# Kernel optimization log

Hardware: AMD Instinct MI355X
Metric: run time of the kernel (lower is better)

The kernel has to match this reference:

```python
import jax, jax.numpy as jnp
import numpy as np

NUM_QUANTIZERS = 8
CODEBOOK_SIZE = 4096
DIM = 128
BATCH = 8
SEQ = 4096


def setup_inputs() -> dict:
    key = jax.random.key(0)
    k1, k2 = jax.random.split(key)
    x = jax.random.normal(k1, (BATCH, DIM, SEQ), dtype=jnp.float32)
    codebooks = jax.random.normal(k2, (NUM_QUANTIZERS, CODEBOOK_SIZE, DIM), dtype=jnp.float32)
    return {"x": x, "codebooks": codebooks}


def _rvq(x_bnc, codebooks):
    """Residual VQ: sequential per-stage nearest-codebook quantization.

    x_bnc: [b, n, d]; codebooks: [Q, K, d].
    Returns quantized [b, n, d], indices [b, n, Q], loss scalar.
    """
    residual = x_bnc
    quantized_out = jnp.zeros_like(x_bnc)
    all_indices = []
    all_losses = []
    Q = codebooks.shape[0]
    for q in range(Q):
        cb = codebooks[q]                                   # [K, d]
        # squared-euclidean distances: ||r||^2 - 2 r.c + ||c||^2  -> [b, n, K]
        r_sq = jnp.sum(residual * residual, axis=-1, keepdims=True)
        c_sq = jnp.sum(cb * cb, axis=-1)
        dots = jnp.einsum('bnd,kd->bnk', residual, cb)
        dist = r_sq - 2.0 * dots + c_sq
        idx = jnp.argmin(dist, axis=-1)                      # [b, n]
        quant = cb[idx]                                      # [b, n, d] gather
        # straight-through estimator (grad flows to residual, not codebook)
        quant_st = residual + jax.lax.stop_gradient(quant - residual)
        quantized_out = quantized_out + quant_st
        # commitment loss (codebook is EMA-updated, so detach the quantized side)
        all_losses.append(jnp.mean((jax.lax.stop_gradient(quant) - residual) ** 2))
        residual = residual - jax.lax.stop_gradient(quant)
        all_indices.append(idx)
    indices = jnp.stack(all_indices, axis=-1)                # [b, n, Q]
    loss = jnp.mean(jnp.stack(all_losses))
    return quantized_out, indices, loss


def reference(x, codebooks):
    # encode(): 'b c n -> b n c', quantize, 'b n c -> b c n'
    x_bnc = jnp.transpose(x, (0, 2, 1))
    quant, indices, loss = _rvq(x_bnc, codebooks)
    out = jnp.transpose(quant, (0, 2, 1))                    # [b, c, n]
    return out, indices, loss
```

## Files before the change

kernel.cpp:

```cpp
#include <hip/hip_runtime.h>

typedef _Float16 half8 __attribute__((ext_vector_type(8)));
typedef float    float4v __attribute__((ext_vector_type(4)));

#define NQ 8
#define KCODES 4096
#define DIMS 128
#define BATCH 8
#define SEQ 4096
#define ROWS (BATCH*SEQ)
#define TM 64
#define NBLK (ROWS/TM)
#define RESPAD 132
#define CANDW 96
#define CANDPAD 100
#define OUT_ELEMS (BATCH*DIMS*SEQ)
#define IDX_ELEMS (BATCH*SEQ*NQ)
#define LOSS_DIV (1.0f/33554432.0f)
#define FRAG_HALVES ((size_t)NQ*4*256*64*8)
#define SBIAS 384.0f
#define WIN 2.0f

__device__ __forceinline__ unsigned umax_(unsigned a, unsigned b){ return a>b?a:b; }
__device__ __forceinline__ unsigned umin_(unsigned a, unsigned b){ return a<b?a:b; }

__global__ void prep_csq(const float* __restrict__ cb, float* __restrict__ csq,
                         float* __restrict__ cinit) {
    int c = blockIdx.x * 256 + threadIdx.x;
    const float4* p = (const float4*)(cb + (size_t)c * DIMS);
    float s = 0.f;
#pragma unroll
    for (int i = 0; i < 32; ++i) {
        float4 v = p[i];
        s += v.x * v.x + v.y * v.y + v.z * v.z + v.w * v.w;
    }
    csq[c] = s;
    cinit[c] = SBIAS - 0.5f * s;
}

__global__ void prep_frags(const float* __restrict__ cb, _Float16* __restrict__ bhi,
                           float* __restrict__ loss_accum) {
    int g = blockIdx.x * 256 + threadIdx.x;
    if (g == 0) loss_accum[0] = 0.f;
    int lane = g & 63;
    int nt   = (g >> 6) & 255;
    int kb   = (g >> 14) & 3;
    int q    = g >> 16;
    int code = nt * 16 + (lane & 15);
    int k0   = kb * 32 + ((lane >> 4) * 8);
    const float* src = cb + ((size_t)q * KCODES + code) * DIMS + k0;
    float4 v0 = *(const float4*)(src);
    float4 v1 = *(const float4*)(src + 4);
    half8 h;
    h[0] = (_Float16)v0.x; h[1] = (_Float16)v0.y; h[2] = (_Float16)v0.z; h[3] = (_Float16)v0.w;
    h[4] = (_Float16)v1.x; h[5] = (_Float16)v1.y; h[6] = (_Float16)v1.z; h[7] = (_Float16)v1.w;
    *(half8*)(bhi + (size_t)g * 8) = h;
}

__device__ __forceinline__ void load_b(const _Float16* __restrict__ bq,
                                       const float* __restrict__ cinq,
                                       int nt, int lane, half8 (&bh)[4], float& cs) {
#pragma unroll
    for (int kb = 0; kb < 4; ++kb) {
        size_t off = (((size_t)kb * 256 + nt) * 64 + lane) * 8;
        bh[kb] = *(const half8*)(bq + off);
    }
    cs = cinq[nt * 16 + (lane & 15)];
}

__device__ __forceinline__ void compute_tile(int nt, int lane,
        const half8 (&ahi)[4][4], const half8 (&bh)[4], float cs,
        unsigned (&p1)[4][4], unsigned (&p2)[4][4], unsigned (&p3)[4][4]) {
    float4v acc[4];
#pragma unroll
    for (int mt = 0; mt < 4; ++mt) { acc[mt][0] = cs; acc[mt][1] = cs; acc[mt][2] = cs; acc[mt][3] = cs; }
    __builtin_amdgcn_s_setprio(1);
#pragma unroll
    for (int kb = 0; kb < 4; ++kb)
#pragma unroll
        for (int mt = 0; mt < 4; ++mt)
            acc[mt] = __builtin_amdgcn_mfma_f32_16x16x32_f16(ahi[mt][kb], bh[kb], acc[mt], 0, 0, 0);
    __builtin_amdgcn_s_setprio(0);
    unsigned idxv = (unsigned)(nt * 16 + (lane & 15));
#pragma unroll
    for (int mt = 0; mt < 4; ++mt)
#pragma unroll
        for (int r = 0; r < 4; ++r) {
            unsigned p  = (__float_as_uint(acc[mt][r]) & 0xFFFFF000u) | idxv;
            unsigned t1 = umin_(p1[mt][r], p);
            p1[mt][r]   = umax_(p1[mt][r], p);
            unsigned t2 = umin_(p2[mt][r], t1);
            p2[mt][r]   = umax_(p2[mt][r], t1);
            p3[mt][r]   = umax_(p3[mt][r], t2);
        }
}

__launch_bounds__(256, 2)
__global__ void rvq_main(const float* __restrict__ x, const float* __restrict__ cb,
                         const _Float16* __restrict__ bhi,
                         const float* __restrict__ csq, const float* __restrict__ cinit,
                         float* __restrict__ out, float* __restrict__ loss_accum) {
    __shared__ float    res[TM][RESPAD];
    __shared__ unsigned cand[TM][CANDPAD];
    __shared__ float    fbin[TM];
    __shared__ float    red[256];

    int tid  = threadIdx.x;
    int lane = tid & 63;
    int wv   = tid >> 6;
    int r0   = blockIdx.x * TM;
    int b    = r0 >> 12;
    int n0   = r0 & (SEQ - 1);
    const float* xb = x + (size_t)b * DIMS * SEQ + n0;

    {
        int d = tid >> 1, half = (tid & 1) * 32;
        const float* src = xb + (size_t)d * SEQ + half;
#pragma unroll
        for (int t4 = 0; t4 < 8; ++t4) {
            float4 v = *(const float4*)(src + t4 * 4);
            res[half + t4 * 4 + 0][d] = v.x;
            res[half + t4 * 4 + 1][d] = v.y;
            res[half + t4 * 4 + 2][d] = v.z;
            res[half + t4 * 4 + 3][d] = v.w;
        }
    }

    float lossacc = 0.f;

    for (int q = 0; q < NQ; ++q) {
        __syncthreads();

        half8 ahi[4][4];
#pragma unroll
        for (int mt = 0; mt < 4; ++mt)
#pragma unroll
        for (int kb = 0; kb < 4; ++kb) {
            int row = mt * 16 + (lane & 15);
            int k0  = kb * 32 + (lane >> 4) * 8;
            float4 v0 = *(const float4*)&res[row][k0];
            float4 v1 = *(const float4*)&res[row][k0 + 4];
            half8 h;
            h[0] = (_Float16)v0.x; h[1] = (_Float16)v0.y; h[2] = (_Float16)v0.z; h[3] = (_Float16)v0.w;
            h[4] = (_Float16)v1.x; h[5] = (_Float16)v1.y; h[6] = (_Float16)v1.z; h[7] = (_Float16)v1.w;
            ahi[mt][kb] = h;
        }

        const _Float16* bq   = bhi + (size_t)q * (4 * 256 * 64 * 8);
        const float*    cinq = cinit + q * KCODES;
        const float*    csqq = csq + q * KCODES;

        unsigned p1[4][4], p2[4][4], p3[4][4];
#pragma unroll
        for (int mt = 0; mt < 4; ++mt)
#pragma unroll
        for (int r = 0; r < 4; ++r) { p1[mt][r] = 0u; p2[mt][r] = 0u; p3[mt][r] = 0u; }

        int ntBase = wv * 64;
        half8 bh0[4], bh1[4];
        float cs0, cs1;
        load_b(bq, cinq, ntBase, lane, bh0, cs0);

        if (wv & 1) {
            float4v accD[4];
#pragma unroll
            for (int mt = 0; mt < 4; ++mt) { accD[mt][0] = cs0; accD[mt][1] = cs0; accD[mt][2] = cs0; accD[mt][3] = cs0; }
            __builtin_amdgcn_s_setprio(1);
#pragma unroll
            for (int kb = 0; kb < 3; ++kb)
#pragma unroll
                for (int mt = 0; mt < 4; ++mt)
                    accD[mt] = __builtin_amdgcn_mfma_f32_16x16x32_f16(ahi[mt][kb], bh0[kb], accD[mt], 0, 0, 0);
            __builtin_amdgcn_s_setprio(0);
            lossacc = fmaf(0.0f, (accD[0][0] + accD[1][0]) + (accD[2][0] + accD[3][0]), lossacc);
        }

        for (int i = 0; i < 64; i += 2) {
            load_b(bq, cinq, ntBase + i + 1, lane, bh1, cs1);
            compute_tile(ntBase + i, lane, ahi, bh0, cs0, p1, p2, p3);
            load_b(bq, cinq, ntBase + ((i + 2) & 63), lane, bh0, cs0);
            compute_tile(ntBase + i + 1, lane, ahi, bh1, cs1, p1, p2, p3);
        }

#pragma unroll
        for (int mt = 0; mt < 4; ++mt)
#pragma unroll
        for (int r = 0; r < 4; ++r) {
            unsigned a1 = p1[mt][r], a2 = p2[mt][r], a3 = p3[mt][r];
            unsigned b1 = (unsigned)__shfl_xor((int)a1, 1, 64);
            unsigned b2 = (unsigned)__shfl_xor((int)a2, 1, 64);
            unsigned b3 = (unsigned)__shfl_xor((int)a3, 1, 64);
            unsigned h  = umax_(a1, b1);
            unsigned l  = umin_(a1, b1);
            unsigned y  = umax_(a2, b2);
            unsigned n2 = umax_(l, y);
            unsigned n3 = umax_(umin_(l, y), umax_(a3, b3));
            if ((lane & 1) == 0) {
                int row = mt * 16 + (lane >> 4) * 4 + r;
                int col = wv * 24 + ((lane & 15) >> 1) * 3;
                cand[row][col]     = h;
                cand[row][col + 1] = n2;
                cand[row][col + 2] = n3;
            }
        }
        __syncthreads();

        {
            int row = tid >> 2, s = tid & 3;
            const unsigned* cp = &cand[row][s * 24];
            unsigned m = 0;
#pragma unroll
            for (int k = 0; k < 24; ++k) m = umax_(m, cp[k]);
            m = umax_(m, (unsigned)__shfl_xor((int)m, 1, 64));
            m = umax_(m, (unsigned)__shfl_xor((int)m, 2, 64));
            float thr = __uint_as_float(m) - WIN;
            float bk = -3.4e38f;
            int   bi = KCODES;
            const float4* rv = (const float4*)&res[row][0];
            for (int k = 0; k < 24; ++k) {
                unsigned e = cp[k];
                if (__uint_as_float(e) >= thr) {
                    int idx = (int)(e & 0xFFFu);
                    const float4* cv = (const float4*)(cb + ((size_t)q * KCODES + idx) * DIMS);
                    float acc = 0.f;
#pragma unroll
                    for (int j = 0; j < 32; ++j) {
                        float4 c4 = cv[j];
                        float4 r4 = rv[j];
                        acc = fmaf(r4.x, c4.x, acc);
                        acc = fmaf(r4.y, c4.y, acc);
                        acc = fmaf(r4.z, c4.z, acc);
                        acc = fmaf(r4.w, c4.w, acc);
                    }
                    float key = acc - 0.5f * csqq[idx];
                    if (key > bk || (key == bk && idx < bi)) { bk = key; bi = idx; }
                }
            }
#pragma unroll
            for (int mask = 1; mask <= 2; mask <<= 1) {
                float ok = __shfl_xor(bk, mask, 64);
                int   oi = __shfl_xor(bi, mask, 64);
                if (ok > bk || (ok == bk && oi < bi)) { bk = ok; bi = oi; }
            }
            if (s == 0) {
                fbin[row] = (float)bi;
                out[OUT_ELEMS + (size_t)(r0 + row) * NQ + q] = (float)bi;
            }
        }
        __syncthreads();

        {
            int row = tid >> 2, j = tid & 3;
            int bi = (int)fbin[row];
            const float* cv = cb + ((size_t)q * KCODES + bi) * DIMS + j * 4;
            float* rp = &res[row][j * 4];
#pragma unroll
            for (int t = 0; t < 8; ++t) {
                float4 c4 = *(const float4*)(cv + t * 16);
                float4 r4 = *(const float4*)(rp + t * 16);
                r4.x -= c4.x; lossacc = fmaf(r4.x, r4.x, lossacc);
                r4.y -= c4.y; lossacc = fmaf(r4.y, r4.y, lossacc);
                r4.z -= c4.z; lossacc = fmaf(r4.z, r4.z, lossacc);
                r4.w -= c4.w; lossacc = fmaf(r4.w, r4.w, lossacc);
                *(float4*)(rp + t * 16) = r4;
            }
        }
    }

    __syncthreads();
    red[tid] = lossacc;
    __syncthreads();
    for (int s = 128; s > 0; s >>= 1) {
        if (tid < s) red[tid] += red[tid + s];
        __syncthreads();
    }
    if (tid == 0) atomicAdd(loss_accum, red[0]);

    {
        int d = tid >> 1, half = (tid & 1) * 32;
        const float* src = xb + (size_t)d * SEQ + half;
        float* dst = out + (size_t)b * DIMS * SEQ + (size_t)d * SEQ + n0 + half;
#pragma unroll
        for (int t4 = 0; t4 < 8; ++t4) {
            float4 v = *(const float4*)(src + t4 * 4);
            v.x -= res[half + t4 * 4 + 0][d];
            v.y -= res[half + t4 * 4 + 1][d];
            v.z -= res[half + t4 * 4 + 2][d];
            v.w -= res[half + t4 * 4 + 3][d];
            *(float4*)(dst + t4 * 4) = v;
        }
    }
}

__global__ void finish_loss(const float* __restrict__ loss_accum, float* __restrict__ out) {
    out[OUT_ELEMS + IDX_ELEMS] = loss_accum[0] * LOSS_DIV;
}

extern "C" void kernel_launch(void* const* d_in, const int* in_sizes, int n_in,
                              void* d_out, int out_size, void* d_ws, size_t ws_size,
                              hipStream_t stream) {
    const float* x  = (const float*)d_in[0];
    const float* cb = (const float*)d_in[1];
    float* out = (float*)d_out;
    char*  ws  = (char*)d_ws;

    float*     loss_accum = (float*)ws;
    float*     csq   = (float*)(ws + 256);
    float*     cinit = (float*)(ws + 256 + 131072);
    _Float16*  bhi   = (_Float16*)(ws + 256 + 262144);

    hipLaunchKernelGGL(prep_csq,   dim3(128),  dim3(256), 0, stream, cb, csq, cinit);
    hipLaunchKernelGGL(prep_frags, dim3(2048), dim3(256), 0, stream, cb, bhi, loss_accum);
    hipLaunchKernelGGL(rvq_main,   dim3(NBLK), dim3(256), 0, stream,
                       x, cb, bhi, csq, cinit, out, loss_accum);
    hipLaunchKernelGGL(finish_loss, dim3(1), dim3(1), 0, stream, loss_accum, out);
}
```

Before: 565.9 us.

## Keep top-2 fp16 candidates per lane and raise occupancy to three blocks

```diff
diff --git a/kernel.cpp b/kernel.cpp
--- a/kernel.cpp
+++ b/kernel.cpp
@@ -12,8 +12,7 @@
 #define TM 64
 #define NBLK (ROWS/TM)
 #define RESPAD 132
-#define CANDW 96
-#define CANDPAD 100
+#define CANDROW 67
 #define OUT_ELEMS (BATCH*DIMS*SEQ)
 #define IDX_ELEMS (BATCH*SEQ*NQ)
 #define LOSS_DIV (1.0f/33554432.0f)
@@ -70,7 +69,7 @@
 
 __device__ __forceinline__ void compute_tile(int nt, int lane,
         const half8 (&ahi)[4][4], const half8 (&bh)[4], float cs,
-        unsigned (&p1)[4][4], unsigned (&p2)[4][4], unsigned (&p3)[4][4]) {
+        unsigned (&p1)[4][4], unsigned (&p2)[4][4]) {
     float4v acc[4];
 #pragma unroll
     for (int mt = 0; mt < 4; ++mt) { acc[mt][0] = cs; acc[mt][1] = cs; acc[mt][2] = cs; acc[mt][3] = cs; }
@@ -89,19 +88,17 @@
             unsigned p  = (__float_as_uint(acc[mt][r]) & 0xFFFFF000u) | idxv;
             unsigned t1 = umin_(p1[mt][r], p);
             p1[mt][r]   = umax_(p1[mt][r], p);
-            unsigned t2 = umin_(p2[mt][r], t1);
             p2[mt][r]   = umax_(p2[mt][r], t1);
-            p3[mt][r]   = umax_(p3[mt][r], t2);
-        }
-}
-
-__launch_bounds__(256, 2)
+        }
+}
+
+__launch_bounds__(256, 3)
 __global__ void rvq_main(const float* __restrict__ x, const float* __restrict__ cb,
                          const _Float16* __restrict__ bhi,
                          const float* __restrict__ csq, const float* __restrict__ cinit,
                          float* __restrict__ out, float* __restrict__ loss_accum) {
     __shared__ float    res[TM][RESPAD];
-    __shared__ unsigned cand[TM][CANDPAD];
+    __shared__ unsigned cand[TM][CANDROW];
     __shared__ float    fbin[TM];
     __shared__ float    red[256];
 
@@ -150,11 +147,11 @@
         const float*    cinq = cinit + q * KCODES;
         const float*    csqq = csq + q * KCODES;
 
-        unsigned p1[4][4], p2[4][4], p3[4][4];
+        unsigned p1[4][4], p2[4][4];
 #pragma unroll
         for (int mt = 0; mt < 4; ++mt)
 #pragma unroll
-        for (int r = 0; r < 4; ++r) { p1[mt][r] = 0u; p2[mt][r] = 0u; p3[mt][r] = 0u; }
+        for (int r = 0; r < 4; ++r) { p1[mt][r] = 0u; p2[mt][r] = 0u; }
 
         int ntBase = wv * 64;
         half8 bh0[4], bh1[4];
@@ -177,47 +174,42 @@
 
         for (int i = 0; i < 64; i += 2) {
             load_b(bq, cinq, ntBase + i + 1, lane, bh1, cs1);
-            compute_tile(ntBase + i, lane, ahi, bh0, cs0, p1, p2, p3);
+            compute_tile(ntBase + i, lane, ahi, bh0, cs0, p1, p2);
             load_b(bq, cinq, ntBase + ((i + 2) & 63), lane, bh0, cs0);
-            compute_tile(ntBase + i + 1, lane, ahi, bh1, cs1, p1, p2, p3);
+            compute_tile(ntBase + i + 1, lane, ahi, bh1, cs1, p1, p2);
         }
 
 #pragma unroll
         for (int mt = 0; mt < 4; ++mt)
 #pragma unroll
         for (int r = 0; r < 4; ++r) {
-            unsigned a1 = p1[mt][r], a2 = p2[mt][r], a3 = p3[mt][r];
+            unsigned a1 = p1[mt][r], a2 = p2[mt][r];
             unsigned b1 = (unsigned)__shfl_xor((int)a1, 1, 64);
             unsigned b2 = (unsigned)__shfl_xor((int)a2, 1, 64);
-            unsigned b3 = (unsigned)__shfl_xor((int)a3, 1, 64);
-            unsigned h  = umax_(a1, b1);
-            unsigned l  = umin_(a1, b1);
-            unsigned y  = umax_(a2, b2);
-            unsigned n2 = umax_(l, y);
-            unsigned n3 = umax_(umin_(l, y), umax_(a3, b3));
+            unsigned n1 = umax_(a1, b1);
+            unsigned n2 = umax_(umin_(a1, b1), umax_(a2, b2));
             if ((lane & 1) == 0) {
                 int row = mt * 16 + (lane >> 4) * 4 + r;
-                int col = wv * 24 + ((lane & 15) >> 1) * 3;
-                cand[row][col]     = h;
+                int col = wv * 16 + ((lane & 15) >> 1) * 2;
+                cand[row][col]     = n1;
                 cand[row][col + 1] = n2;
-                cand[row][col + 2] = n3;
             }
         }
         __syncthreads();
 
         {
             int row = tid >> 2, s = tid & 3;
-            const unsigned* cp = &cand[row][s * 24];
+            const unsigned* cp = &cand[row][s * 16];
             unsigned m = 0;
 #pragma unroll
-            for (int k = 0; k < 24; ++k) m = umax_(m, cp[k]);
+            for (int k = 0; k < 16; ++k) m = umax_(m, cp[k]);
             m = umax_(m, (unsigned)__shfl_xor((int)m, 1, 64));
             m = umax_(m, (unsigned)__shfl_xor((int)m, 2, 64));
             float thr = __uint_as_float(m) - WIN;
             float bk = -3.4e38f;
             int   bi = KCODES;
             const float4* rv = (const float4*)&res[row][0];
-            for (int k = 0; k < 24; ++k) {
+            for (int k = 0; k < 16; ++k) {
                 unsigned e = cp[k];
                 if (__uint_as_float(e) >= thr) {
                     int idx = (int)(e & 0xFFFu);
@@ -252,17 +244,17 @@
         {
             int row = tid >> 2, j = tid & 3;
             int bi = (int)fbin[row];
-            const float* cv = cb + ((size_t)q * KCODES + bi) * DIMS + j * 4;
-            float* rp = &res[row][j * 4];
+            const float* cv = cb + ((size_t)q * KCODES + bi) * DIMS + j * 32;
+            float* rp = &res[row][j * 32];
 #pragma unroll
             for (int t = 0; t < 8; ++t) {
-                float4 c4 = *(const float4*)(cv + t * 16);
-                float4 r4 = *(const float4*)(rp + t * 16);
+                float4 c4 = *(const float4*)(cv + t * 4);
+                float4 r4 = *(const float4*)(rp + t * 4);
                 r4.x -= c4.x; lossacc = fmaf(r4.x, r4.x, lossacc);
                 r4.y -= c4.y; lossacc = fmaf(r4.y, r4.y, lossacc);
                 r4.z -= c4.z; lossacc = fmaf(r4.z, r4.z, lossacc);
                 r4.w -= c4.w; lossacc = fmaf(r4.w, r4.w, lossacc);
-                *(float4*)(rp + t * 16) = r4;
+                *(float4*)(rp + t * 4) = r4;
             }
         }
     }
```

After: 1.754 ms. 3.1x slower.
